# Kernel tuning notes

Measured on AMD Instinct MI355X. Metric: run time of the kernel, lower is better.

The kernel has to match this reference:

```python
import jax, jax.numpy as jnp
import numpy as np

BATCH, IN, HID, OMID, OUT = 8192, 64, 1024, 128, 1
MAX_ITER = 8
EPS = 1e-3


def setup_inputs() -> dict:
    key = jax.random.key(0)
    ks = jax.random.split(key, 32)
    s_in, s_h = 1.0 / np.sqrt(IN), 1.0 / np.sqrt(HID)
    d = {"x": jax.random.normal(ks[0], (BATCH, IN), jnp.float32)}
    names = ["i", "f", "c", "o"]
    for j, n in enumerate(names):
        d[f"Wx{n}"] = jax.random.uniform(ks[1 + 4 * j], (HID, IN), jnp.float32, -s_in, s_in)
        d[f"bx{n}"] = jax.random.uniform(ks[2 + 4 * j], (HID,), jnp.float32, -s_in, s_in)
        d[f"Wh{n}"] = jax.random.uniform(ks[3 + 4 * j], (HID, HID), jnp.float32, -s_h, s_h)
        d[f"bh{n}"] = jax.random.uniform(ks[4 + 4 * j], (HID,), jnp.float32, -s_h, s_h)
    d["W_halt"] = jax.random.uniform(ks[20], (1, HID), jnp.float32, -s_h, s_h)
    d["b_halt"] = jax.random.uniform(ks[21], (1,), jnp.float32, -s_h, s_h)
    d["W1"] = jax.random.uniform(ks[22], (OMID, HID), jnp.float32, -s_h, s_h)
    d["b1"] = jax.random.uniform(ks[23], (OMID,), jnp.float32, -s_h, s_h)
    s_m = 1.0 / np.sqrt(OMID)
    d["W2"] = jax.random.uniform(ks[24], (OUT, OMID), jnp.float32, -s_m, s_m)
    d["b2"] = jax.random.uniform(ks[25], (OUT,), jnp.float32, -s_m, s_m)
    return d


def _act_forward(x, Wxi, bxi, Whi, bhi, Wxf, bxf, Whf, bhf, Wxc, bxc, Whc, bhc,
                 Wxo, bxo, Who, bho, W_halt, b_halt, W1, b1, W2, b2):
    B = x.shape[0]
    state0 = jnp.zeros((B, HID), x.dtype)
    cell0 = jnp.zeros((B, HID), x.dtype)
    p0 = jnp.zeros((B,), x.dtype)
    active0 = jnp.ones((B,), bool)

    def step(carry, t):
        state, cell, p_sum, active = carry
        # four LSTM-style gates (computed dense; masked update == torch's gather/scatter)
        i_g = jax.nn.sigmoid(x @ Wxi.T + bxi + state @ Whi.T + bhi)
        f_g = jax.nn.sigmoid(x @ Wxf.T + bxf + state @ Whf.T + bhf)
        c_g = jnp.tanh(x @ Wxc.T + bxc + state @ Whc.T + bhc)
        o_g = jax.nn.sigmoid(x @ Wxo.T + bxo + state @ Who.T + bho)
        am = active[:, None]
        cell = jnp.where(am, f_g * cell + i_g * c_g, cell)
        state = jnp.where(am, o_g * jnp.tanh(cell), state)
        out = jax.nn.sigmoid(jax.nn.relu(state @ W1.T + b1) @ W2.T + b2)  # (B, OUT)
        h = jax.nn.sigmoid(state @ W_halt.T + b_halt)[:, 0]               # (B,)
        p_new = p_sum + h
        last = t == MAX_ITER - 1
        finished = active & ((p_new >= 1.0 - EPS) | last)
        halt_rec = jnp.where(finished, 1.0 - p_sum, jnp.where(active, h, 0.0))
        p_sum = jnp.where(finished, 1.0, jnp.where(active, p_new, p_sum))
        out_rec = jnp.where(am, out, 0.0)
        active = active & ~finished
        return (state, cell, p_sum, active), (out_rec, halt_rec)

    _, (outs, halts) = jax.lax.scan(step, (state0, cell0, p0, active0), jnp.arange(MAX_ITER))
    # outs: (T, B, OUT), halts: (T, B); final = sum_t out_t * p_halt_t
    return jnp.einsum("tbo,tb->bo", outs, halts)


def reference(x, Wxi, bxi, Whi, bhi, Wxf, bxf, Whf, bhf, Wxc, bxc, Whc, bhc,
              Wxo, bxo, Who, bho, W_halt, b_halt, W1, b1, W2, b2):
    return _act_forward(x, Wxi, bxi, Whi, bhi, Wxf, bxf, Whf, bhf, Wxc, bxc, Whc, bhc,
                        Wxo, bxo, Who, bho, W_halt, b_halt, W1, b1, W2, b2)
```

## Files before the change

### kernel.cpp

```cpp
#include <hip/hip_runtime.h>
#include <hip/hip_bf16.h>

#define BATCH 8192
#define IN_DIM 64
#define HID 1024
#define KTOT 1088
#define NGATES 4096
#define OMID 128
#define NP 256
#define MAX_ITER 8

#define TM 128
#define TN 128
#define TK 64
#define GYD 16
#define TAILB 64

typedef __attribute__((ext_vector_type(8))) short short8;
typedef __attribute__((ext_vector_type(4))) float float4v;

__device__ __forceinline__ float bf2f(short s) {
    union { float f; unsigned u; } v; v.u = ((unsigned)(unsigned short)s) << 16; return v.f;
}
__device__ __forceinline__ short f2bf(float f) {
    union { float f; unsigned u; } v; v.f = f;
    unsigned r = v.u + 0x7fff + ((v.u >> 16) & 1);
    return (short)(r >> 16);
}
__device__ __forceinline__ float sigmoidf_(float x) {
    float xc = fminf(fmaxf(x, -30.f), 30.f);
    return 1.f / (1.f + __expf(-xc));
}
__device__ __forceinline__ float tanhf_(float x) {
    float xc = fminf(fmaxf(x, -15.f), 15.f);
    float e = __expf(2.f * xc);
    return (e - 1.f) / (e + 1.f);
}
__device__ __forceinline__ int aload(const int* p) {
    return __hip_atomic_load((int*)p, __ATOMIC_RELAXED, __HIP_MEMORY_SCOPE_AGENT);
}
__device__ __forceinline__ void astore(int* p, int v) {
    __hip_atomic_store(p, v, __ATOMIC_RELAXED, __HIP_MEMORY_SCOPE_AGENT);
}

__device__ __forceinline__ void gbar(int* bar, int phase, int tid) {
    __syncthreads();
    if (tid == 0) {
        __threadfence();
        __hip_atomic_fetch_add(bar, 1, __ATOMIC_ACQ_REL, __HIP_MEMORY_SCOPE_AGENT);
        while (aload(bar) < TAILB * phase)
            __builtin_amdgcn_s_sleep(8);
        __threadfence();
    }
    __syncthreads();
}

__device__ __forceinline__ void gates_epilogue(
    const float4v (&acc)[4][4], int m0, int bx, int wave, int lane, int first,
    const float* __restrict__ bias_g, float* __restrict__ cell,
    short* __restrict__ Sout, const int* __restrict__ ridx, int n_act)
{
    const int wm = wave & 1, wn = wave >> 1;
    const int colq = lane & 15, q = lane >> 4;
    const int G = bx * 2 + wn;
    const int h = G * 16 + colq;
    const float bi  = bias_g[G * 64 +  0 + colq];
    const float bff = bias_g[G * 64 + 16 + colq];
    const float bc  = bias_g[G * 64 + 32 + colq];
    const float bo  = bias_g[G * 64 + 48 + colq];
#pragma unroll
    for (int i = 0; i < 4; ++i) {
        const int pbase = m0 + wm * 64 + i * 16 + q * 4;
#pragma unroll
        for (int r = 0; r < 4; ++r) {
            const int pos = pbase + r;
            if (pos < n_act) {
                const int row = ridx[pos];
                const float ig = sigmoidf_(acc[i][0][r] + bi);
                const float fg = sigmoidf_(acc[i][1][r] + bff);
                const float cg = tanhf_(acc[i][2][r] + bc);
                const float og = sigmoidf_(acc[i][3][r] + bo);
                const size_t ci = (size_t)row * HID + h;
                const float c = first ? (ig * cg) : (fg * cell[ci] + ig * cg);
                cell[ci] = c;
                Sout[(size_t)row * HID + h] = f2bf(og * tanhf_(c));
            }
        }
    }
}

__global__ __launch_bounds__(256, 2) void gates_k(
    const short* __restrict__ S, const short* __restrict__ XB,
    const short* __restrict__ B,
    const float* __restrict__ bias_g, int nK, int hidK, int first,
    float* __restrict__ cell, short* __restrict__ Sout,
    const int* __restrict__ ridx, const int* __restrict__ cnt, int t)
{
    __shared__ short Bs[TN * TK];
    __shared__ short As0[TM * TK];
    __shared__ short As1[TM * TK];
    const int n_act = cnt[t];
    const int tid  = threadIdx.x;
    const int wave = tid >> 6, lane = tid & 63;
    const int wm = wave & 1, wn = wave >> 1;
    const int colq = lane & 15, q = lane >> 4;
    const int lrow8 = lane >> 3;
    const int lk    = (((lane & 7) ^ lrow8) * 8);
    const int n0 = blockIdx.x * TN;

    int aoff[4][2], boff[4][2];
#pragma unroll
    for (int i = 0; i < 4; ++i) {
        const int Ra = wm * 64 + i * 16 + colq;
        const int Rb = wn * 64 + i * 16 + colq;
#pragma unroll
        for (int c2 = 0; c2 < 2; ++c2) {
            const int C = q + 4 * c2;
            aoff[i][c2] = Ra * TK + ((C ^ (Ra & 7)) << 3);
            boff[i][c2] = Rb * TK + ((C ^ (Rb & 7)) << 3);
        }
    }

    for (int by0 = blockIdx.y; by0 * TM < n_act; by0 += 2 * (int)gridDim.y) {
        const int by1 = by0 + gridDim.y;
        const bool dual = (by1 * TM < n_act);
        const int m0 = by0 * TM, m1 = by1 * TM;

        float4v acc0[4][4], acc1[4][4];
#pragma unroll
        for (int i = 0; i < 4; ++i)
#pragma unroll
            for (int j = 0; j < 4; ++j) { acc0[i][j] = (float4v)0.f; acc1[i][j] = (float4v)0.f; }

        const short* gaS0[4];
        const short* gaS1[4];
        const short* gaX0[4];
        const short* gaX1[4];
        const short* gb[4];
#pragma unroll
        for (int it = 0; it < 4; ++it) {
            const int rr = (wave * 4 + it) * 8;
            const int r0 = ridx[m0 + rr + lrow8];
            const int r1 = dual ? ridx[m1 + rr + lrow8] : r0;
            gaS0[it] = S + (size_t)r0 * HID + lk;
            gaS1[it] = S + (size_t)r1 * HID + lk;
            gaX0[it] = XB + (size_t)r0 * IN_DIM + lk;
            gaX1[it] = XB + (size_t)r1 * IN_DIM + lk;
            gb[it]   = B + (size_t)(n0 + rr + lrow8) * KTOT + lk;
        }

        for (int ki = 0; ki < nK; ++ki) {
            const bool fromS = (ki * TK < hidK);
#pragma unroll
            for (int it = 0; it < 4; ++it) {
                const int rr = (wave * 4 + it) * 8;
                __builtin_amdgcn_global_load_lds(
                    (const __attribute__((address_space(1))) void*)gb[it],
                    (__attribute__((address_space(3))) void*)(Bs + rr * TK), 16, 0, 0);
                const short* a0 = fromS ? gaS0[it] : gaX0[it];
                __builtin_amdgcn_global_load_lds(
                    (const __attribute__((address_space(1))) void*)a0,
                    (__attribute__((address_space(3))) void*)(As0 + rr * TK), 16, 0, 0);
                if (dual) {
                    const short* a1 = fromS ? gaS1[it] : gaX1[it];
                    __builtin_amdgcn_global_load_lds(
                        (const __attribute__((address_space(1))) void*)a1,
                        (__attribute__((address_space(3))) void*)(As1 + rr * TK), 16, 0, 0);
                }
                gaS0[it] += TK; gaS1[it] += TK; gb[it] += TK;
            }
            __syncthreads();
#pragma unroll
            for (int c2 = 0; c2 < 2; ++c2) {
                short8 bf[4], af0[4], af1[4];
#pragma unroll
                for (int i = 0; i < 4; ++i) {
                    bf[i]  = *(const short8*)(Bs  + boff[i][c2]);
                    af0[i] = *(const short8*)(As0 + aoff[i][c2]);
                    af1[i] = *(const short8*)(As1 + aoff[i][c2]);
                }
#pragma unroll
                for (int i = 0; i < 4; ++i)
#pragma unroll
                    for (int j = 0; j < 4; ++j) {
                        acc0[i][j] = __builtin_amdgcn_mfma_f32_16x16x32_bf16(af0[i], bf[j], acc0[i][j], 0, 0, 0);
                        acc1[i][j] = __builtin_amdgcn_mfma_f32_16x16x32_bf16(af1[i], bf[j], acc1[i][j], 0, 0, 0);
                    }
            }
            __syncthreads();
        }

        gates_epilogue(acc0, m0, blockIdx.x, wave, lane, first, bias_g, cell, Sout, ridx, n_act);
        if (dual)
            gates_epilogue(acc1, m1, blockIdx.x, wave, lane, first, bias_g, cell, Sout, ridx, n_act);
        __syncthreads();
    }
}

__device__ __forceinline__ void gates_tile(
    short* As, short* Bs, int tid,
    const short* __restrict__ S, const short* __restrict__ XB,
    const short* __restrict__ B,
    const float* __restrict__ bias_g,
    float* __restrict__ cell, short* __restrict__ Sout,
    const int* __restrict__ ridx, int n_act, int m0, int bx)
{
    const int wave = tid >> 6, lane = tid & 63;
    const int wm = wave & 1, wn = wave >> 1;
    const int colq = lane & 15, q = lane >> 4;
    const int lrow8 = lane >> 3;
    const int lk    = (((lane & 7) ^ lrow8) * 8);
    const int n0 = bx * TN;

    int aoff[4][2], boff[4][2];
#pragma unroll
    for (int i = 0; i < 4; ++i) {
        const int Ra = wm * 64 + i * 16 + colq;
        const int Rb = wn * 64 + i * 16 + colq;
#pragma unroll
        for (int c2 = 0; c2 < 2; ++c2) {
            const int C = q + 4 * c2;
            aoff[i][c2] = Ra * TK + ((C ^ (Ra & 7)) << 3);
            boff[i][c2] = Rb * TK + ((C ^ (Rb & 7)) << 3);
        }
    }

    float4v acc[4][4];
#pragma unroll
    for (int i = 0; i < 4; ++i)
#pragma unroll
        for (int j = 0; j < 4; ++j) acc[i][j] = (float4v)0.f;

    const short* gaS[4];
    const short* gaX[4];
    const short* gb[4];
#pragma unroll
    for (int it = 0; it < 4; ++it) {
        const int rr = (wave * 4 + it) * 8;
        const int r0 = ridx[m0 + rr + lrow8];
        gaS[it] = S + (size_t)r0 * HID + lk;
        gaX[it] = XB + (size_t)r0 * IN_DIM + lk;
        gb[it]  = B + (size_t)(n0 + rr + lrow8) * KTOT + lk;
    }

    for (int ki = 0; ki < KTOT / TK; ++ki) {
        const bool fromS = (ki * TK < HID);
#pragma unroll
        for (int it = 0; it < 4; ++it) {
            const int rr = (wave * 4 + it) * 8;
            const short* a0 = fromS ? gaS[it] : gaX[it];
            __builtin_amdgcn_global_load_lds(
                (const __attribute__((address_space(1))) void*)a0,
                (__attribute__((address_space(3))) void*)(As + rr * TK), 16, 0, 0);
            __builtin_amdgcn_global_load_lds(
                (const __attribute__((address_space(1))) void*)gb[it],
                (__attribute__((address_space(3))) void*)(Bs + rr * TK), 16, 0, 0);
            gaS[it] += TK; gb[it] += TK;
        }
        __syncthreads();
#pragma unroll
        for (int c2 = 0; c2 < 2; ++c2) {
            short8 af[4], bf[4];
#pragma unroll
            for (int i = 0; i < 4; ++i) {
                af[i] = *(const short8*)(As + aoff[i][c2]);
                bf[i] = *(const short8*)(Bs + boff[i][c2]);
            }
#pragma unroll
            for (int i = 0; i < 4; ++i)
#pragma unroll
                for (int j = 0; j < 4; ++j)
                    acc[i][j] = __builtin_amdgcn_mfma_f32_16x16x32_bf16(af[i], bf[j], acc[i][j], 0, 0, 0);
        }
        __syncthreads();
    }

    gates_epilogue(acc, m0, bx, wave, lane, 0, bias_g, cell, Sout, ridx, n_act);
    __syncthreads();
}

__device__ __forceinline__ void midfin_tile(
    short* As, short* Bs, int tid,
    const short* __restrict__ Snew, const short* __restrict__ P,
    const float* __restrict__ bias_p, const float* __restrict__ W_halt,
    const float* __restrict__ W2, const float* __restrict__ b2,
    float* __restrict__ outp, float* __restrict__ p_sum,
    const int* __restrict__ rprev, int* __restrict__ rnext,
    int* __restrict__ cnt, int t, int m0, int n_act)
{
    const int wave = tid >> 6, lane = tid & 63;
    const int wm = wave & 1, wn = wave >> 1;
    const int colq = lane & 15, q = lane >> 4;
    const int lrow8 = lane >> 3;
    const int lk    = (((lane & 7) ^ lrow8) * 8);

    float4v acc[4][4];
#pragma unroll
    for (int i = 0; i < 4; ++i)
#pragma unroll
        for (int j = 0; j < 4; ++j) acc[i][j] = (float4v)0.f;

    const short* ga[4];
    const short* gb[4];
#pragma unroll
    for (int it = 0; it < 4; ++it) {
        const int rr = (wave * 4 + it) * 8;
        ga[it] = Snew + (size_t)rprev[m0 + rr + lrow8] * HID + lk;
        gb[it] = P + (size_t)(rr + lrow8) * HID + lk;
    }
    int aoff[4][2], boff[4][2];
#pragma unroll
    for (int i = 0; i < 4; ++i) {
        const int Ra = wm * 64 + i * 16 + colq;
        const int Rb = wn * 64 + i * 16 + colq;
#pragma unroll
        for (int c2 = 0; c2 < 2; ++c2) {
            const int C = q + 4 * c2;
            aoff[i][c2] = Ra * TK + ((C ^ (Ra & 7)) << 3);
            boff[i][c2] = Rb * TK + ((C ^ (Rb & 7)) << 3);
        }
    }

    for (int k0 = 0; k0 < HID; k0 += TK) {
#pragma unroll
        for (int it = 0; it < 4; ++it) {
            const int rr = (wave * 4 + it) * 8;
            __builtin_amdgcn_global_load_lds(
                (const __attribute__((address_space(1))) void*)ga[it],
                (__attribute__((address_space(3))) void*)(As + rr * TK), 16, 0, 0);
            __builtin_amdgcn_global_load_lds(
                (const __attribute__((address_space(1))) void*)gb[it],
                (__attribute__((address_space(3))) void*)(Bs + rr * TK), 16, 0, 0);
            ga[it] += TK; gb[it] += TK;
        }
        __syncthreads();
#pragma unroll
        for (int c2 = 0; c2 < 2; ++c2) {
            short8 af[4], bf[4];
#pragma unroll
            for (int i = 0; i < 4; ++i) {
                af[i] = *(const short8*)(As + aoff[i][c2]);
                bf[i] = *(const short8*)(Bs + boff[i][c2]);
            }
#pragma unroll
            for (int i = 0; i < 4; ++i)
#pragma unroll
                for (int j = 0; j < 4; ++j)
                    acc[i][j] = __builtin_amdgcn_mfma_f32_16x16x32_bf16(af[i], bf[j], acc[i][j], 0, 0, 0);
        }
        __syncthreads();
    }

    float* red  = (float*)As;
    float* hbuf = ((float*)As) + 256;

    for (int s = 0; s < 32; ++s) {
        const int lr = wave * 32 + s;
        const int row = rprev[m0 + lr];
        const short* Ar = Snew + (size_t)row * HID + lane * 16;
        const short8 v0 = *(const short8*)Ar;
        const short8 v1 = *(const short8*)(Ar + 8);
        const float* Wh = W_halt + lane * 16;
        float hv = 0.f;
#pragma unroll
        for (int e = 0; e < 8; ++e) hv += bf2f(v0[e]) * Wh[e];
#pragma unroll
        for (int e = 0; e < 8; ++e) hv += bf2f(v1[e]) * Wh[8 + e];
#pragma unroll
        for (int o = 32; o > 0; o >>= 1) hv += __shfl_down(hv, o);
        if (lane == 0) hbuf[lr] = hv;
    }

    float pr[4][4];
#pragma unroll
    for (int i = 0; i < 4; ++i)
#pragma unroll
        for (int r = 0; r < 4; ++r) pr[i][r] = 0.f;
#pragma unroll
    for (int j = 0; j < 4; ++j) {
        const int col = wn * 64 + j * 16 + colq;
        const float b = bias_p[col];
        const float w2 = W2[col];
#pragma unroll
        for (int i = 0; i < 4; ++i)
#pragma unroll
            for (int r = 0; r < 4; ++r)
                pr[i][r] += fmaxf(acc[i][j][r] + b, 0.f) * w2;
    }
#pragma unroll
    for (int i = 0; i < 4; ++i)
#pragma unroll
        for (int r = 0; r < 4; ++r) {
            float v = pr[i][r];
            v += __shfl_down(v, 8, 16);
            v += __shfl_down(v, 4, 16);
            v += __shfl_down(v, 2, 16);
            v += __shfl_down(v, 1, 16);
            if (colq == 0)
                red[((((wn * 2) + wm) * 4 + i) * 4 + q) * 4 + r] = v;
        }
    __syncthreads();

    if (tid < TM) {
        const int pos = m0 + tid;
        if (pos < n_act) {
            const int lwm = tid >> 6, i = (tid >> 4) & 3, lq = (tid >> 2) & 3, r = tid & 3;
            const float odot = red[((lwm * 4 + i) * 4 + lq) * 4 + r]
                             + red[(((2 + lwm) * 4 + i) * 4 + lq) * 4 + r];
            const int row = rprev[pos];
            const float ov = sigmoidf_(odot + b2[0]);
            const float h  = sigmoidf_(hbuf[tid] + bias_p[OMID]);
            const float ps = p_sum[row];
            const float pn = ps + h;
            const bool fin = (pn >= 1.f - 1e-3f) || (t == MAX_ITER - 1);
            const float halt = fin ? (1.f - ps) : h;
            outp[row] += ov * halt;
            p_sum[row] = fin ? 1.f : pn;
            if (!fin) {
                const int d = atomicAdd(&cnt[t + 1], 1);
                astore(&rnext[d], row);
            }
        }
    }
    __syncthreads();
}

__global__ __launch_bounds__(256) void midfin_k(
    const short* __restrict__ Snew, const short* __restrict__ P,
    const float* __restrict__ bias_p, const float* __restrict__ W_halt,
    const float* __restrict__ W2, const float* __restrict__ b2,
    float* __restrict__ outp, float* __restrict__ p_sum,
    const int* __restrict__ rprev, int* __restrict__ rnext,
    int* __restrict__ cnt, int t)
{
    __shared__ short As[TM * TK];
    __shared__ short Bs[TN * TK];
    const int n_act = cnt[t];
    for (int tile = blockIdx.x; tile * TM < n_act; tile += gridDim.x)
        midfin_tile(As, Bs, threadIdx.x, Snew, P, bias_p, W_halt, W2, b2,
                    outp, p_sum, rprev, rnext, cnt, t, tile * TM, n_act);
}

__global__ __launch_bounds__(256) void tail_k(
    const short* __restrict__ Wg, const float* __restrict__ bias_g,
    const short* __restrict__ P, const float* __restrict__ bias_p,
    const float* __restrict__ W_halt, const float* __restrict__ W2,
    const float* __restrict__ b2,
    short* __restrict__ S0, short* __restrict__ S1,
    const short* __restrict__ XB,
    float* __restrict__ cell, float* __restrict__ outp,
    float* __restrict__ p_sum,
    int* __restrict__ ridx0, int* __restrict__ ridx1,
    int* __restrict__ cnt, int* __restrict__ bar)
{
    __shared__ short As[TM * TK];
    __shared__ short Bs[TN * TK];
    const int tid = threadIdx.x;
    int phase = 0;
    int t = 2;
    while (true) {
        short* Snew = (t & 1) ? S0 : S1;
        const int* rprev = (t & 1) ? ridx1 : ridx0;
        int* rnext = (t & 1) ? ridx0 : ridx1;
        const int n = aload(&cnt[t]);
        for (int tile = blockIdx.x; tile * TM < n; tile += gridDim.x)
            midfin_tile(As, Bs, tid, Snew, P, bias_p, W_halt, W2, b2,
                        outp, p_sum, rprev, rnext, cnt, t, tile * TM, n);
        if (t == MAX_ITER - 1) break;
        ++phase; gbar(bar, phase, tid);
        const int n1 = aload(&cnt[t + 1]);
        if (n1 == 0) break;
        {
            short* Sot = (t & 1) ? S1 : S0;
            const int ntiles = ((n1 + TM - 1) / TM) * (NGATES / TN);
            for (int e = blockIdx.x; e < ntiles; e += gridDim.x)
                gates_tile(As, Bs, tid, Snew, XB, Wg, bias_g, cell, Sot,
                           rnext, n1, (e >> 5) * TM, e & 31);
        }
        ++phase; gbar(bar, phase, tid);
        ++t;
    }
}

#define SETUP_XB    (BATCH * IN_DIM)
#define SETUP_WG    (NGATES * KTOT)
#define SETUP_P     (NP * HID)
#define SETUP_TOT   (SETUP_XB + SETUP_WG + SETUP_P)
__global__ __launch_bounds__(256) void setup_k(
    const float* __restrict__ x,
    const float* __restrict__ Whi, const float* __restrict__ Whf,
    const float* __restrict__ Whc, const float* __restrict__ Who,
    const float* __restrict__ Wxi, const float* __restrict__ Wxf,
    const float* __restrict__ Wxc, const float* __restrict__ Wxo,
    const float* __restrict__ bxi, const float* __restrict__ bhi,
    const float* __restrict__ bxf, const float* __restrict__ bhf,
    const float* __restrict__ bxc, const float* __restrict__ bhc,
    const float* __restrict__ bxo, const float* __restrict__ bho,
    const float* __restrict__ W1, const float* __restrict__ b1,
    const float* __restrict__ W_halt, const float* __restrict__ b_halt,
    short* __restrict__ XB,
    float* __restrict__ p_sum,
    int* __restrict__ ridx0, int* __restrict__ ridx1, int* __restrict__ cnt,
    int* __restrict__ bar, float* __restrict__ outp,
    short* __restrict__ Wg, float* __restrict__ bias_g,
    short* __restrict__ P, float* __restrict__ bias_p)
{
    int idx = blockIdx.x * 256 + threadIdx.x;
    if (idx < SETUP_XB) {
        const int row = idx >> 6, k = idx & 63;
        XB[idx] = f2bf(x[idx]);
        if (k == 0) {
            p_sum[row] = 0.f;
            outp[row] = 0.f;
            ridx0[row] = row;
            ridx1[row] = 0;
        }
        if (row == 0 && k <= MAX_ITER) cnt[k] = (k == 0) ? BATCH : 0;
        if (row == 1 && k == 0) bar[0] = 0;
        return;
    }
    idx -= SETUP_XB;
    if (idx < SETUP_WG) {
        const int n = idx / KTOT, k = idx - n * KTOT;
        const int G = n >> 6, g = (n >> 4) & 3, q = n & 15;
        const int h = G * 16 + q;
        const float* Wh = (g == 0) ? Whi : (g == 1) ? Whf : (g == 2) ? Whc : Who;
        const float* Wx = (g == 0) ? Wxi : (g == 1) ? Wxf : (g == 2) ? Wxc : Wxo;
        const float v = (k < HID) ? Wh[h * HID + k] : Wx[h * IN_DIM + (k - HID)];
        Wg[idx] = f2bf(v);
        if (k == 0) {
            const float* bx = (g == 0) ? bxi : (g == 1) ? bxf : (g == 2) ? bxc : bxo;
            const float* bh = (g == 0) ? bhi : (g == 1) ? bhf : (g == 2) ? bhc : bho;
            bias_g[n] = bx[h] + bh[h];
        }
        return;
    }
    idx -= SETUP_WG;
    if (idx < SETUP_P) {
        const int n = idx >> 10, k = idx & 1023;
        const float v = (n < OMID) ? W1[n * HID + k] : (n == OMID ? W_halt[k] : 0.f);
        P[idx] = f2bf(v);
        if (k == 0) bias_p[n] = (n < OMID) ? b1[n] : (n == OMID ? b_halt[0] : 0.f);
    }
}

extern "C" void kernel_launch(void* const* d_in, const int* in_sizes, int n_in,
                              void* d_out, int out_size, void* d_ws, size_t ws_size,
                              hipStream_t stream) {
    const float* x    = (const float*)d_in[0];
    const float* Wxi  = (const float*)d_in[1];
    const float* bxi  = (const float*)d_in[2];
    const float* Whi  = (const float*)d_in[3];
    const float* bhi  = (const float*)d_in[4];
    const float* Wxf  = (const float*)d_in[5];
    const float* bxf  = (const float*)d_in[6];
    const float* Whf  = (const float*)d_in[7];
    const float* bhf  = (const float*)d_in[8];
    const float* Wxc  = (const float*)d_in[9];
    const float* bxc  = (const float*)d_in[10];
    const float* Whc  = (const float*)d_in[11];
    const float* bhc  = (const float*)d_in[12];
    const float* Wxo  = (const float*)d_in[13];
    const float* bxo  = (const float*)d_in[14];
    const float* Who  = (const float*)d_in[15];
    const float* bho  = (const float*)d_in[16];
    const float* W_halt = (const float*)d_in[17];
    const float* b_halt = (const float*)d_in[18];
    const float* W1   = (const float*)d_in[19];
    const float* b1   = (const float*)d_in[20];
    const float* W2   = (const float*)d_in[21];
    const float* b2   = (const float*)d_in[22];

    char* p = (char*)d_ws;
    auto carve = [&](size_t bytes) { char* r = p; p += (bytes + 255) & ~(size_t)255; return r; };
    short* S0     = (short*)carve((size_t)BATCH * HID * 2);
    short* S1     = (short*)carve((size_t)BATCH * HID * 2);
    short* XB     = (short*)carve((size_t)BATCH * IN_DIM * 2);
    short* Wg     = (short*)carve((size_t)NGATES * KTOT * 2);
    float* bias_g = (float*)carve((size_t)NGATES * 4);
    short* P      = (short*)carve((size_t)NP * HID * 2);
    float* bias_p = (float*)carve((size_t)NP * 4);
    float* cell   = (float*)carve((size_t)BATCH * HID * 4);
    float* p_sum  = (float*)carve((size_t)BATCH * 4);
    int*   ridx0  = (int*)carve((size_t)BATCH * 4);
    int*   ridx1  = (int*)carve((size_t)BATCH * 4);
    int*   cnt    = (int*)carve((size_t)(MAX_ITER + 1) * 4);
    int*   bar    = (int*)carve(256);
    float* outp   = (float*)d_out;

    setup_k<<<(SETUP_TOT + 255) / 256, 256, 0, stream>>>(
        x, Whi, Whf, Whc, Who, Wxi, Wxf, Wxc, Wxo,
        bxi, bhi, bxf, bhf, bxc, bhc, bxo, bho,
        W1, b1, W_halt, b_halt,
        XB, p_sum, ridx0, ridx1, cnt, bar, outp,
        Wg, bias_g, P, bias_p);

    gates_k<<<dim3(NGATES / TN, GYD), 256, 0, stream>>>(
        S0, XB, Wg + HID, bias_g, 1, 0, 1, cell, S1, ridx0, cnt, 0);
    midfin_k<<<64, 256, 0, stream>>>(
        S1, P, bias_p, W_halt, W2, b2, outp, p_sum, ridx0, ridx1, cnt, 0);
    gates_k<<<dim3(NGATES / TN, GYD), 256, 0, stream>>>(
        S1, XB, Wg, bias_g, KTOT / TK, HID, 0, cell, S0, ridx1, cnt, 1);
    midfin_k<<<64, 256, 0, stream>>>(
        S0, P, bias_p, W_halt, W2, b2, outp, p_sum, ridx1, ridx0, cnt, 1);
    gates_k<<<dim3(NGATES / TN, GYD), 256, 0, stream>>>(
        S0, XB, Wg, bias_g, KTOT / TK, HID, 0, cell, S1, ridx0, cnt, 2);
    tail_k<<<TAILB, 256, 0, stream>>>(
        Wg, bias_g, P, bias_p, W_halt, W2, b2,
        S0, S1, XB, cell, outp, p_sum, ridx0, ridx1, cnt, bar);
}
```

Measured before the change: 432.9 us.

## Enlarge gates GEMM tile to 256x256 with double-buffered LDS staging

The gates kernel moves from 128x128 tiles (with optional dual M-tile) on 256-thread blocks to a single 256x256 tile on 512-thread blocks. Each wave now computes 128x64. LDS is double-buffered so the next K-slice loads overlap the MFMA work, and one barrier per K step is removed. The grid shrinks to 16x16 blocks. The larger tile cuts global traffic per FLOP, but it raises register pressure and gives fewer blocks, so occupancy and load balance may suffer. With fewer active rows, the 256-row M-tiles also waste more work.

```diff
diff --git a/kernel.cpp b/kernel.cpp
--- a/kernel.cpp
+++ b/kernel.cpp
@@ -13,7 +13,8 @@
 #define TM 128
 #define TN 128
 #define TK 64
-#define GYD 16
+#define GTM 256
+#define GTN 256
 #define TAILB 64
 
 typedef __attribute__((ext_vector_type(8))) short short8;
@@ -89,111 +90,115 @@
     }
 }
 
-__global__ __launch_bounds__(256, 2) void gates_k(
+__global__ __launch_bounds__(512, 1) void gates_k(
     const short* __restrict__ S, const short* __restrict__ XB,
     const short* __restrict__ B,
     const float* __restrict__ bias_g, int nK, int hidK, int first,
     float* __restrict__ cell, short* __restrict__ Sout,
     const int* __restrict__ ridx, const int* __restrict__ cnt, int t)
 {
-    __shared__ short Bs[TN * TK];
-    __shared__ short As0[TM * TK];
-    __shared__ short As1[TM * TK];
+    __shared__ short As[2][GTM * TK];
+    __shared__ short Bs[2][GTN * TK];
     const int n_act = cnt[t];
     const int tid  = threadIdx.x;
     const int wave = tid >> 6, lane = tid & 63;
-    const int wm = wave & 1, wn = wave >> 1;
+    const int wm2 = wave >> 2, wn4 = wave & 3;
     const int colq = lane & 15, q = lane >> 4;
     const int lrow8 = lane >> 3;
     const int lk    = (((lane & 7) ^ lrow8) * 8);
-    const int n0 = blockIdx.x * TN;
-
-    int aoff[4][2], boff[4][2];
-#pragma unroll
-    for (int i = 0; i < 4; ++i) {
-        const int Ra = wm * 64 + i * 16 + colq;
-        const int Rb = wn * 64 + i * 16 + colq;
-#pragma unroll
-        for (int c2 = 0; c2 < 2; ++c2) {
-            const int C = q + 4 * c2;
-            aoff[i][c2] = Ra * TK + ((C ^ (Ra & 7)) << 3);
-            boff[i][c2] = Rb * TK + ((C ^ (Rb & 7)) << 3);
-        }
-    }
-
-    for (int by0 = blockIdx.y; by0 * TM < n_act; by0 += 2 * (int)gridDim.y) {
-        const int by1 = by0 + gridDim.y;
-        const bool dual = (by1 * TM < n_act);
-        const int m0 = by0 * TM, m1 = by1 * TM;
-
-        float4v acc0[4][4], acc1[4][4];
-#pragma unroll
-        for (int i = 0; i < 4; ++i)
-#pragma unroll
-            for (int j = 0; j < 4; ++j) { acc0[i][j] = (float4v)0.f; acc1[i][j] = (float4v)0.f; }
-
-        const short* gaS0[4];
-        const short* gaS1[4];
-        const short* gaX0[4];
-        const short* gaX1[4];
+    const int n0 = blockIdx.x * GTN;
+    const int xq = colq & 7;
+    const int abase = (wm2 * 128 + colq) * TK;
+    const int bbase = (wn4 * 64  + colq) * TK;
+
+    for (int by = blockIdx.y; by * GTM < n_act; by += gridDim.y) {
+        const int m0 = by * GTM;
+
+        int rows_[4];
         const short* gb[4];
 #pragma unroll
         for (int it = 0; it < 4; ++it) {
-            const int rr = (wave * 4 + it) * 8;
-            const int r0 = ridx[m0 + rr + lrow8];
-            const int r1 = dual ? ridx[m1 + rr + lrow8] : r0;
-            gaS0[it] = S + (size_t)r0 * HID + lk;
-            gaS1[it] = S + (size_t)r1 * HID + lk;
-            gaX0[it] = XB + (size_t)r0 * IN_DIM + lk;
-            gaX1[it] = XB + (size_t)r1 * IN_DIM + lk;
-            gb[it]   = B + (size_t)(n0 + rr + lrow8) * KTOT + lk;
-        }
+            const int rr = wave * 32 + it * 8 + lrow8;
+            rows_[it] = ridx[m0 + rr];
+            gb[it] = B + (size_t)(n0 + rr) * KTOT + lk;
+        }
+
+        float4v acc[8][4];
+#pragma unroll
+        for (int i = 0; i < 8; ++i)
+#pragma unroll
+            for (int j = 0; j < 4; ++j) acc[i][j] = (float4v)0.f;
+
+        auto stage = [&](int ki, int buf) {
+            const int kk = ki * TK;
+            const bool fromS = (kk < hidK);
+#pragma unroll
+            for (int it = 0; it < 4; ++it) {
+                const int dst = (wave * 32 + it * 8) * TK;
+                const short* sa = fromS
+                    ? (S  + (size_t)rows_[it] * HID    + kk + lk)
+                    : (XB + (size_t)rows_[it] * IN_DIM + lk);
+                __builtin_amdgcn_global_load_lds(
+                    (const __attribute__((address_space(1))) void*)sa,
+                    (__attribute__((address_space(3))) void*)(As[buf] + dst), 16, 0, 0);
+                __builtin_amdgcn_global_load_lds(
+                    (const __attribute__((address_space(1))) void*)(gb[it] + kk),
+                    (__attribute__((address_space(3))) void*)(Bs[buf] + dst), 16, 0, 0);
+            }
+        };
+
+        stage(0, 0);
+        __syncthreads();
 
         for (int ki = 0; ki < nK; ++ki) {
-            const bool fromS = (ki * TK < hidK);
-#pragma unroll
-            for (int it = 0; it < 4; ++it) {
-                const int rr = (wave * 4 + it) * 8;
-                __builtin_amdgcn_global_load_lds(
-                    (const __attribute__((address_space(1))) void*)gb[it],
-                    (__attribute__((address_space(3))) void*)(Bs + rr * TK), 16, 0, 0);
-                const short* a0 = fromS ? gaS0[it] : gaX0[it];
-                __builtin_amdgcn_global_load_lds(
-                    (const __attribute__((address_space(1))) void*)a0,
-                    (__attribute__((address_space(3))) void*)(As0 + rr * TK), 16, 0, 0);
-                if (dual) {
-                    const short* a1 = fromS ? gaS1[it] : gaX1[it];
-                    __builtin_amdgcn_global_load_lds(
-                        (const __attribute__((address_space(1))) void*)a1,
-                        (__attribute__((address_space(3))) void*)(As1 + rr * TK), 16, 0, 0);
-                }
-                gaS0[it] += TK; gaS1[it] += TK; gb[it] += TK;
+            const int cur = ki & 1;
+            if (ki + 1 < nK) stage(ki + 1, cur ^ 1);
+            const short* Ac = As[cur];
+            const short* Bc = Bs[cur];
+#pragma unroll
+            for (int c2 = 0; c2 < 2; ++c2) {
+                const int xt = ((q + 4 * c2) ^ xq) << 3;
+                short8 af[8], bf[4];
+#pragma unroll
+                for (int i = 0; i < 8; ++i)
+                    af[i] = *(const short8*)(Ac + abase + i * (16 * TK) + xt);
+#pragma unroll
+                for (int j = 0; j < 4; ++j)
+                    bf[j] = *(const short8*)(Bc + bbase + j * (16 * TK) + xt);
+#pragma unroll
+                for (int i = 0; i < 8; ++i)
+#pragma unroll
+                    for (int j = 0; j < 4; ++j)
+                        acc[i][j] = __builtin_amdgcn_mfma_f32_16x16x32_bf16(af[i], bf[j], acc[i][j], 0, 0, 0);
             }
             __syncthreads();
-#pragma unroll
-            for (int c2 = 0; c2 < 2; ++c2) {
-                short8 bf[4], af0[4], af1[4];
-#pragma unroll
-                for (int i = 0; i < 4; ++i) {
-                    bf[i]  = *(const short8*)(Bs  + boff[i][c2]);
-                    af0[i] = *(const short8*)(As0 + aoff[i][c2]);
-                    af1[i] = *(const short8*)(As1 + aoff[i][c2]);
+        }
+
+        const int G = blockIdx.x * 4 + wn4;
+        const int h = G * 16 + colq;
+        const float bi  = bias_g[G * 64 +  0 + colq];
+        const float bff = bias_g[G * 64 + 16 + colq];
+        const float bc  = bias_g[G * 64 + 32 + colq];
+        const float bo  = bias_g[G * 64 + 48 + colq];
+#pragma unroll
+        for (int i = 0; i < 8; ++i) {
+            const int pbase = m0 + wm2 * 128 + i * 16 + q * 4;
+#pragma unroll
+            for (int r = 0; r < 4; ++r) {
+                const int pos = pbase + r;
+                if (pos < n_act) {
+                    const int row = ridx[pos];
+                    const float ig = sigmoidf_(acc[i][0][r] + bi);
+                    const float fg = sigmoidf_(acc[i][1][r] + bff);
+                    const float cg = tanhf_(acc[i][2][r] + bc);
+                    const float og = sigmoidf_(acc[i][3][r] + bo);
+                    const size_t ci = (size_t)row * HID + h;
+                    const float c = first ? (ig * cg) : (fg * cell[ci] + ig * cg);
+                    cell[ci] = c;
+                    Sout[(size_t)row * HID + h] = f2bf(og * tanhf_(c));
                 }
-#pragma unroll
-                for (int i = 0; i < 4; ++i)
-#pragma unroll
-                    for (int j = 0; j < 4; ++j) {
-                        acc0[i][j] = __builtin_amdgcn_mfma_f32_16x16x32_bf16(af0[i], bf[j], acc0[i][j], 0, 0, 0);
-                        acc1[i][j] = __builtin_amdgcn_mfma_f32_16x16x32_bf16(af1[i], bf[j], acc1[i][j], 0, 0, 0);
-                    }
             }
-            __syncthreads();
-        }
-
-        gates_epilogue(acc0, m0, blockIdx.x, wave, lane, first, bias_g, cell, Sout, ridx, n_act);
-        if (dual)
-            gates_epilogue(acc1, m1, blockIdx.x, wave, lane, first, bias_g, cell, Sout, ridx, n_act);
-        __syncthreads();
+        }
     }
 }
 
@@ -595,15 +600,15 @@
         XB, p_sum, ridx0, ridx1, cnt, bar, outp,
         Wg, bias_g, P, bias_p);
 
-    gates_k<<<dim3(NGATES / TN, GYD), 256, 0, stream>>>(
+    gates_k<<<dim3(NGATES / GTN, 16), 512, 0, stream>>>(
         S0, XB, Wg + HID, bias_g, 1, 0, 1, cell, S1, ridx0, cnt, 0);
     midfin_k<<<64, 256, 0, stream>>>(
         S1, P, bias_p, W_halt, W2, b2, outp, p_sum, ridx0, ridx1, cnt, 0);
-    gates_k<<<dim3(NGATES / TN, GYD), 256, 0, stream>>>(
+    gates_k<<<dim3(NGATES / GTN, 16), 512, 0, stream>>>(
         S1, XB, Wg, bias_g, KTOT / TK, HID, 0, cell, S0, ridx1, cnt, 1);
     midfin_k<<<64, 256, 0, stream>>>(
         S0, P, bias_p, W_halt, W2, b2, outp, p_sum, ridx1, ridx0, cnt, 1);
-    gates_k<<<dim3(NGATES / TN, GYD), 256, 0, stream>>>(
+    gates_k<<<dim3(NGATES / GTN, 16), 512, 0, stream>>>(
         S0, XB, Wg, bias_g, KTOT / TK, HID, 0, cell, S1, ridx0, cnt, 2);
     tail_k<<<TAILB, 256, 0, stream>>>(
         Wg, bias_g, P, bias_p, W_halt, W2, b2,
```

After: 471.5 us. 1.09x slower.
